# Performance work log

Measured on AMD Instinct MI355X. Metric: run time of the kernel, lower is better.

Reference implementation:

```python
import math
import jax, jax.numpy as jnp
import numpy as np

B, S, D, H = 4, 2048, 768, 12
HD = D // H  # 64


def setup_inputs() -> dict:
    key = jax.random.key(0)
    ks = jax.random.split(key, 10)
    sc = 0.02
    return {
        "hidden_states": jax.random.normal(ks[0], (B, S, D), dtype=jnp.float32),
        "attention_mask": jax.random.randint(ks[1], (1, H, S, S), 0, 2).astype(jnp.bool_),
        "q_w": jax.random.normal(ks[2], (D, D), dtype=jnp.float32) * sc,
        "q_b": jax.random.normal(ks[3], (D,), dtype=jnp.float32) * sc,
        "k_w": jax.random.normal(ks[4], (D, D), dtype=jnp.float32) * sc,
        "k_b": jax.random.normal(ks[5], (D,), dtype=jnp.float32) * sc,
        "v_w": jax.random.normal(ks[6], (D, D), dtype=jnp.float32) * sc,
        "v_b": jax.random.normal(ks[7], (D,), dtype=jnp.float32) * sc,
        "out_w": jax.random.normal(ks[8], (D, D), dtype=jnp.float32) * sc,
        "out_b": jax.random.normal(ks[9], (D,), dtype=jnp.float32) * sc,
    }


def _split_heads(x):
    # [B, S, D] -> [B, H, S, HD]
    b, s, _ = x.shape
    return x.reshape(b, s, H, HD).transpose(0, 2, 1, 3)


def reference(hidden_states, attention_mask, q_w, q_b, k_w, k_b, v_w, v_b, out_w, out_b):
    q = _split_heads(hidden_states @ q_w.T + q_b)
    k = _split_heads(hidden_states @ k_w.T + k_b)
    v = _split_heads(hidden_states @ v_w.T + v_b)
    scores = jnp.einsum("bhqd,bhkd->bhqk", q, k) / math.sqrt(HD)
    # prune_mode, before softmax: masked_fill(~mask, -inf)
    scores = jnp.where(attention_mask, scores, -jnp.inf)
    probs = jax.nn.softmax(scores, axis=-1)  # [B, H, S, S]
    ctx = jnp.einsum("bhqk,bhkd->bhqd", probs, v)
    ctx = ctx.transpose(0, 2, 1, 3).reshape(hidden_states.shape[0], -1, D)
    return ctx @ out_w.T + out_b
```

## Files before the change

kernel.cpp:

```cpp
#include <hip/hip_runtime.h>
#include <hip/hip_bf16.h>

#define B_ 4
#define S_ 2048
#define D_ 768
#define H_ 12
#define HD_ 64

typedef __attribute__((ext_vector_type(8))) short bf16x8;
typedef __attribute__((ext_vector_type(4))) float floatx4;

#define QSCALE 0.18033688011112042f

__device__ __forceinline__ unsigned short f2bf(float x) {
    union { float f; unsigned int u; } v; v.f = x;
    unsigned int r = v.u + 0x7fffu + ((v.u >> 16) & 1u);
    return (unsigned short)(r >> 16);
}

__device__ __forceinline__ unsigned int pk2bf(float a, float b) {
    __hip_bfloat162 h = __float22bfloat162_rn(make_float2(a, b));
    unsigned int u;
    __builtin_memcpy(&u, &h, 4);
    return u;
}

__device__ __forceinline__ void gload_lds16(const void* g, void* l) {
    __builtin_amdgcn_global_load_lds(
        (const __attribute__((address_space(1))) unsigned int*)g,
        (__attribute__((address_space(3))) unsigned int*)l, 16, 0, 0);
}

__global__ void prep(const float* __restrict__ hs,
                     const float* __restrict__ w0, const float* __restrict__ w1,
                     const float* __restrict__ w2, const float* __restrict__ w3,
                     const int* __restrict__ mask,
                     unsigned short* __restrict__ Xb,
                     unsigned short* __restrict__ Wb,
                     unsigned long long* __restrict__ bits) {
    int bid = blockIdx.x;
    int t = threadIdx.x;
    if (bid < 6144) {
        int i = bid * 256 + t;
        float4 f = ((const float4*)hs)[i];
        ushort4 o;
        o.x = f2bf(f.x); o.y = f2bf(f.y); o.z = f2bf(f.z); o.w = f2bf(f.w);
        ((ushort4*)Xb)[i] = o;
    } else if (bid < 8448) {
        int q = bid - 6144;
        int wid = q / 576;
        const float* src = (wid == 0) ? w0 : (wid == 1) ? w1 : (wid == 2) ? w2 : w3;
        unsigned short* d = Wb + (size_t)wid * 589824;
        int i = (q - wid * 576) * 256 + t;
        float4 f = ((const float4*)src)[i];
        ushort4 o;
        o.x = f2bf(f.x); o.y = f2bf(f.y); o.z = f2bf(f.z); o.w = f2bf(f.w);
        ((ushort4*)d)[i] = o;
    } else {
        size_t gw = ((size_t)(bid - 8448) * 256 + t) >> 6;
        int lane = t & 63;
        size_t base = gw * 256;
        unsigned long long b0 = __ballot(mask[base + lane] != 0);
        unsigned long long b1 = __ballot(mask[base + 64 + lane] != 0);
        unsigned long long b2 = __ballot(mask[base + 128 + lane] != 0);
        unsigned long long b3 = __ballot(mask[base + 192 + lane] != 0);
        if (lane == 0) {
            bits[gw * 4 + 0] = b0; bits[gw * 4 + 1] = b1;
            bits[gw * 4 + 2] = b2; bits[gw * 4 + 3] = b3;
        }
    }
}

__global__ __launch_bounds__(256) void qkv_gemm(
    const unsigned short* __restrict__ Xb,
    const unsigned short* __restrict__ Wq, const unsigned short* __restrict__ Wk,
    const unsigned short* __restrict__ Wv,
    const float* __restrict__ bq, const float* __restrict__ bk,
    const float* __restrict__ bv,
    unsigned short* __restrict__ Qo, unsigned short* __restrict__ Ko,
    unsigned short* __restrict__ Vo)
{
    const int z = blockIdx.z;
    const unsigned short* W = (z == 0) ? Wq : (z == 1) ? Wk : Wv;
    const float* bias = (z == 0) ? bq : (z == 1) ? bk : bv;
    unsigned short* Out = (z == 0) ? Qo : (z == 1) ? Ko : Vo;
    const float scale = (z == 0) ? QSCALE : 1.0f;

    const int m0 = blockIdx.x * 128;
    const int n0 = blockIdx.y * 128;

    __shared__ alignas(16) unsigned short SMall[16384];
    unsigned short* SM = SMall;

    const int t = threadIdx.x;
    const int lane = t & 63, w = t >> 6;
    const int c = lane & 15, quad = lane >> 4;
    const int wm = (w & 1) * 64, wn = (w >> 1) * 64;

    const int srowq = lane >> 2, sc8 = (lane & 3) * 8;

    floatx4 acc[4][4];
#pragma unroll
    for (int i = 0; i < 4; i++)
#pragma unroll
        for (int j = 0; j < 4; j++) acc[i][j] = (floatx4){0.f, 0.f, 0.f, 0.f};

#pragma unroll
    for (int i = 0; i < 2; i++) {
        int chunk = i * 4 + w;
        int row = chunk * 16 + srowq;
        gload_lds16(&Xb[(size_t)(m0 + row) * 768 + sc8], &SMall[chunk * 512]);
        gload_lds16(&W [(size_t)(n0 + row) * 768 + sc8], &SMall[4096 + chunk * 512]);
    }

    for (int it = 0; it < 24; it++) {
        const int cur = it & 1;
        __syncthreads();
        if (it + 1 < 24) {
            int k1 = (it + 1) * 32;
#pragma unroll
            for (int i = 0; i < 2; i++) {
                int chunk = i * 4 + w;
                int row = chunk * 16 + srowq;
                gload_lds16(&Xb[(size_t)(m0 + row) * 768 + k1 + sc8],
                            &SMall[(cur ^ 1) * 8192 + chunk * 512]);
                gload_lds16(&W [(size_t)(n0 + row) * 768 + k1 + sc8],
                            &SMall[(cur ^ 1) * 8192 + 4096 + chunk * 512]);
            }
        }
        const unsigned short* As = &SMall[cur * 8192];
        const unsigned short* Bs = As + 4096;
        bf16x8 a[4], b[4];
#pragma unroll
        for (int i = 0; i < 4; i++)
            a[i] = *(const bf16x8*)&As[(wm + i * 16 + c) * 32 + quad * 8];
#pragma unroll
        for (int j = 0; j < 4; j++)
            b[j] = *(const bf16x8*)&Bs[(wn + j * 16 + c) * 32 + quad * 8];
#pragma unroll
        for (int i = 0; i < 4; i++)
#pragma unroll
            for (int j = 0; j < 4; j++)
                acc[i][j] = __builtin_amdgcn_mfma_f32_16x16x32_bf16(
                    a[i], b[j], acc[i][j], 0, 0, 0);
    }
    __syncthreads();

    const int bb = m0 >> 11, ssb = m0 & 2047;
    if (z == 2) {
#pragma unroll
        for (int half = 0; half < 2; half++) {
            if ((w >> 1) == half) {
#pragma unroll
                for (int j = 0; j < 4; j++) {
                    int n_l = j * 16 + c;
                    float bias_n = bias[n0 + half * 64 + n_l];
#pragma unroll
                    for (int i = 0; i < 4; i++) {
#pragma unroll
                        for (int r = 0; r < 4; r++) {
                            int m = wm + i * 16 + quad * 4 + r;
                            int ms = m ^ (c << 3);
                            SM[n_l * 128 + ms] = f2bf(acc[i][j][r] + bias_n);
                        }
                    }
                }
            }
            __syncthreads();
#pragma unroll
            for (int rb = 0; rb < 2; rb++) {
                int n_l = (t >> 3) + rb * 32;
                int ch = t & 7;
                int n_abs = n0 + half * 64 + n_l;
                int hh = n_abs >> 6, dd = n_abs & 63;
                unsigned short* dst =
                    Out + (((size_t)(bb * H_ + hh)) * 64 + dd) * S_ + ssb;
#pragma unroll
                for (int p = 0; p < 2; p++) {
                    int mc = ch + p * 8;
                    uint4 v = *(const uint4*)&SM[n_l * 128 + ((mc ^ (n_l & 15)) * 8)];
                    *(uint4*)&dst[mc * 8] = v;
                }
            }
            __syncthreads();
        }
    } else {
#pragma unroll
        for (int half = 0; half < 2; half++) {
            if ((w >> 1) == half) {
#pragma unroll
                for (int j = 0; j < 4; j++) {
                    float bias_n = bias[n0 + half * 64 + j * 16 + c];
#pragma unroll
                    for (int i = 0; i < 4; i++) {
#pragma unroll
                        for (int r = 0; r < 4; r++) {
                            int m = wm + i * 16 + quad * 4 + r;
                            int chunk = (j * 2 + (c >> 3)) ^ ((m >> 1) & 7);
                            SM[m * 64 + chunk * 8 + (c & 7)] =
                                f2bf((acc[i][j][r] + bias_n) * scale);
                        }
                    }
                }
            }
            __syncthreads();
            {
                int hh = (n0 >> 6) + half;
                unsigned short* dst =
                    Out + ((size_t)(bb * H_ + hh) * S_ + ssb) * 64;
#pragma unroll
                for (int i = 0; i < 4; i++) {
                    int idx = i * 256 + t;
                    int m = idx >> 3, ch = idx & 7;
                    uint4 v = *(const uint4*)&SM[m * 64 + ((ch ^ ((m >> 1) & 7)) * 8)];
                    *(uint4*)&dst[(size_t)m * 64 + ch * 8] = v;
                }
            }
            __syncthreads();
        }
    }
}

__global__ __launch_bounds__(256) void out_gemm(
    const unsigned short* __restrict__ Cb, const unsigned short* __restrict__ Wo,
    const float* __restrict__ bo, float* __restrict__ out)
{
    const int m0 = blockIdx.x * 64;
    const int n0 = blockIdx.y * 128;

    __shared__ alignas(16) unsigned short SMall[12288];

    const int t = threadIdx.x;
    const int lane = t & 63, w = t >> 6;
    const int c = lane & 15, quad = lane >> 4;
    const int wm = (w & 1) * 32, wn = (w >> 1) * 64;

    const int arow = w * 16 + (lane >> 2);
    const int brow0 = (lane >> 2);
    const int sc8 = (lane & 3) * 8;

    floatx4 acc[2][4];
#pragma unroll
    for (int i = 0; i < 2; i++)
#pragma unroll
        for (int j = 0; j < 4; j++) acc[i][j] = (floatx4){0.f, 0.f, 0.f, 0.f};

    gload_lds16(&Cb[(size_t)(m0 + arow) * 768 + sc8], &SMall[w * 512]);
#pragma unroll
    for (int i = 0; i < 2; i++) {
        int chunk = i * 4 + w;
        gload_lds16(&Wo[(size_t)(n0 + chunk * 16 + brow0) * 768 + sc8],
                    &SMall[2048 + chunk * 512]);
    }

    for (int it = 0; it < 24; it++) {
        const int cur = it & 1;
        __syncthreads();
        if (it + 1 < 24) {
            int k1 = (it + 1) * 32;
            gload_lds16(&Cb[(size_t)(m0 + arow) * 768 + k1 + sc8],
                        &SMall[(cur ^ 1) * 6144 + w * 512]);
#pragma unroll
            for (int i = 0; i < 2; i++) {
                int chunk = i * 4 + w;
                gload_lds16(&Wo[(size_t)(n0 + chunk * 16 + brow0) * 768 + k1 + sc8],
                            &SMall[(cur ^ 1) * 6144 + 2048 + chunk * 512]);
            }
        }
        const unsigned short* As = &SMall[cur * 6144];
        const unsigned short* Bs = As + 2048;
        bf16x8 a[2], b[4];
#pragma unroll
        for (int i = 0; i < 2; i++)
            a[i] = *(const bf16x8*)&As[(wm + i * 16 + c) * 32 + quad * 8];
#pragma unroll
        for (int j = 0; j < 4; j++)
            b[j] = *(const bf16x8*)&Bs[(wn + j * 16 + c) * 32 + quad * 8];
#pragma unroll
        for (int i = 0; i < 2; i++)
#pragma unroll
            for (int j = 0; j < 4; j++)
                acc[i][j] = __builtin_amdgcn_mfma_f32_16x16x32_bf16(
                    a[i], b[j], acc[i][j], 0, 0, 0);
    }
    __syncthreads();

    float* SMf = (float*)SMall;
#pragma unroll
    for (int qtr = 0; qtr < 4; qtr++) {
        if ((w >> 1) == (qtr >> 1)) {
#pragma unroll
            for (int jj = 0; jj < 2; jj++) {
                int j = (qtr & 1) * 2 + jj;
                float bias_n = bo[n0 + wn + j * 16 + c];
                int chunk = jj * 4 + (c >> 2);
#pragma unroll
                for (int i = 0; i < 2; i++) {
#pragma unroll
                    for (int r = 0; r < 4; r++) {
                        int m = wm + i * 16 + quad * 4 + r;
                        SMf[m * 32 + ((chunk ^ (m & 7)) * 4) + (c & 3)] =
                            acc[i][j][r] + bias_n;
                    }
                }
            }
        }
        __syncthreads();
#pragma unroll
        for (int i = 0; i < 2; i++) {
            int idx = i * 256 + t;
            int m = idx >> 3, ch = idx & 7;
            float4 v = *(const float4*)&SMf[m * 32 + ((ch ^ (m & 7)) * 4)];
            *(float4*)&out[(size_t)(m0 + m) * 768 + n0 + qtr * 32 + ch * 4] = v;
        }
        __syncthreads();
    }
}

__global__ __launch_bounds__(256) void attn(
    const unsigned short* __restrict__ Q, const unsigned short* __restrict__ K,
    const unsigned short* __restrict__ Vt,
    const unsigned long long* __restrict__ mbits,
    unsigned short* __restrict__ ctx)
{
    const int lin = blockIdx.y * 16 + blockIdx.x;
    const int nn = (lin & 7) * 96 + (lin >> 3);
    const int qt = nn & 15;
    const int bh = nn >> 4;
    const int b = bh / H_, h = bh % H_;

    const unsigned short* Qp = Q + (size_t)bh * S_ * 64 + (size_t)qt * 128 * 64;
    const unsigned short* Kp = K + (size_t)bh * S_ * 64;
    const unsigned short* Vp = Vt + (size_t)bh * 64 * S_;

    __shared__ alignas(16) unsigned short Ks[2][64 * 64];
    __shared__ alignas(16) unsigned short Vs[2][64 * 64];
    __shared__ alignas(16) unsigned short Ps[4][16 * 64];

    const int t = threadIdx.x;
    const int lane = t & 63, w = t >> 6;
    const int c = lane & 15, quad = lane >> 4;

    bf16x8 aq[2][2];
#pragma unroll
    for (int st = 0; st < 2; st++) {
        aq[st][0] = *(const bf16x8*)&Qp[(size_t)(w * 32 + st * 16 + c) * 64 + quad * 8];
        aq[st][1] = *(const bf16x8*)&Qp[(size_t)(w * 32 + st * 16 + c) * 64 + 32 + quad * 8];
    }

    const unsigned long long* mrow =
        mbits + ((size_t)h * S_ + qt * 128 + w * 32 + quad * 4) * (S_ / 64);

    floatx4 acc_o[2][4];
#pragma unroll
    for (int st = 0; st < 2; st++)
#pragma unroll
        for (int i = 0; i < 4; i++) acc_o[st][i] = (floatx4){0.f, 0.f, 0.f, 0.f};
    float lp[2][4] = {{0.f, 0.f, 0.f, 0.f}, {0.f, 0.f, 0.f, 0.f}};

    const int srow = (lane >> 3);
    const int rc0 = ((quad     ) ^ (c & 7)) * 8;
    const int rc1 = ((quad + 4) ^ (c & 7)) * 8;

    const int psr0 = c * 64 + ((quad ^ (c & 7)) << 3);
    const int psr1 = c * 64 + (((quad + 4) ^ (c & 7)) << 3);

#pragma unroll
    for (int i = 0; i < 2; i++) {
        int chunk = i * 4 + w;
        int row = chunk * 8 + srow;
        int col8 = (((lane & 7) ^ ((row >> 2) & 7))) * 8;
        gload_lds16(&Kp[(size_t)row * 64 + col8], &Ks[0][chunk * 512]);
        gload_lds16(&Vp[(size_t)row * S_ + col8], &Vs[0][chunk * 512]);
    }

    for (int kt = 0; kt < S_ / 64; kt++) {
        const int cur = kt & 1;
        __syncthreads();

        unsigned long long mk[2][4];
#pragma unroll
        for (int st = 0; st < 2; st++)
#pragma unroll
            for (int r = 0; r < 4; r++)
                mk[st][r] = mrow[st * 512 + r * 32 + kt];

        if (kt + 1 < S_ / 64) {
#pragma unroll
            for (int i = 0; i < 2; i++) {
                int chunk = i * 4 + w;
                int row = chunk * 8 + srow;
                int col8 = (((lane & 7) ^ ((row >> 2) & 7))) * 8;
                gload_lds16(&Kp[(size_t)((kt + 1) * 64 + row) * 64 + col8],
                            &Ks[cur ^ 1][chunk * 512]);
                gload_lds16(&Vp[(size_t)row * S_ + (kt + 1) * 64 + col8],
                            &Vs[cur ^ 1][chunk * 512]);
            }
        }

        unsigned int pk1[2][4];
#pragma unroll
        for (int p = 0; p < 2; p++) {
            floatx4 zz[2][2];
            zz[0][0] = (floatx4){0.f, 0.f, 0.f, 0.f};
            zz[0][1] = (floatx4){0.f, 0.f, 0.f, 0.f};
            zz[1][0] = (floatx4){0.f, 0.f, 0.f, 0.f};
            zz[1][1] = (floatx4){0.f, 0.f, 0.f, 0.f};
#pragma unroll
            for (int q2 = 0; q2 < 2; q2++) {
                int kr = 4 * c + 2 * p + q2;
                bf16x8 bk0 = *(const bf16x8*)&Ks[cur][kr * 64 + rc0];
                bf16x8 bk1 = *(const bf16x8*)&Ks[cur][kr * 64 + rc1];
                zz[0][q2] = __builtin_amdgcn_mfma_f32_16x16x32_bf16(aq[0][0], bk0, zz[0][q2], 0, 0, 0);
                zz[0][q2] = __builtin_amdgcn_mfma_f32_16x16x32_bf16(aq[0][1], bk1, zz[0][q2], 0, 0, 0);
                zz[1][q2] = __builtin_amdgcn_mfma_f32_16x16x32_bf16(aq[1][0], bk0, zz[1][q2], 0, 0, 0);
                zz[1][q2] = __builtin_amdgcn_mfma_f32_16x16x32_bf16(aq[1][1], bk1, zz[1][q2], 0, 0, 0);
            }

            asm volatile("" ::: "memory");
#pragma unroll
            for (int r = 0; r < 4; r++) {
                unsigned int n2 = (unsigned int)(mk[0][r] >> (4 * c + 2 * p)) & 3u;
                float p0 = (n2 & 1u) ? __builtin_amdgcn_exp2f(zz[0][0][r]) : 0.f;
                float p1 = (n2 & 2u) ? __builtin_amdgcn_exp2f(zz[0][1][r]) : 0.f;
                lp[0][r] += p0 + p1;
                int row = quad * 4 + r;
                *(unsigned int*)&Ps[w][row * 64 + (((c >> 1) ^ (row & 7)) << 3) +
                                       ((c & 1) << 2) + 2 * p] = pk2bf(p0, p1);
            }
#pragma unroll
            for (int r = 0; r < 4; r++) {
                unsigned int n2 = (unsigned int)(mk[1][r] >> (4 * c + 2 * p)) & 3u;
                float p0 = (n2 & 1u) ? __builtin_amdgcn_exp2f(zz[1][0][r]) : 0.f;
                float p1 = (n2 & 2u) ? __builtin_amdgcn_exp2f(zz[1][1][r]) : 0.f;
                lp[1][r] += p0 + p1;
                pk1[p][r] = pk2bf(p0, p1);
            }
            asm volatile("" ::: "memory");
        }

        bf16x8 ap[2][2];
        ap[0][0] = *(const bf16x8*)&Ps[w][psr0];
        ap[0][1] = *(const bf16x8*)&Ps[w][psr1];
        asm volatile("" ::: "memory");
#pragma unroll
        for (int p = 0; p < 2; p++)
#pragma unroll
            for (int r = 0; r < 4; r++) {
                int row = quad * 4 + r;
                *(unsigned int*)&Ps[w][row * 64 + (((c >> 1) ^ (row & 7)) << 3) +
                                       ((c & 1) << 2) + 2 * p] = pk1[p][r];
            }
        asm volatile("" ::: "memory");
        ap[1][0] = *(const bf16x8*)&Ps[w][psr0];
        ap[1][1] = *(const bf16x8*)&Ps[w][psr1];

#pragma unroll
        for (int nt = 0; nt < 4; nt++) {
            int vr = 4 * c + nt;
            bf16x8 bv0 = *(const bf16x8*)&Vs[cur][vr * 64 + rc0];
            bf16x8 bv1 = *(const bf16x8*)&Vs[cur][vr * 64 + rc1];
#pragma unroll
            for (int st = 0; st < 2; st++) {
                acc_o[st][nt] = __builtin_amdgcn_mfma_f32_16x16x32_bf16(ap[st][0], bv0, acc_o[st][nt], 0, 0, 0);
                acc_o[st][nt] = __builtin_amdgcn_mfma_f32_16x16x32_bf16(ap[st][1], bv1, acc_o[st][nt], 0, 0, 0);
            }
        }
    }

#pragma unroll
    for (int st = 0; st < 2; st++)
#pragma unroll
        for (int r = 0; r < 4; r++) {
            float s = lp[st][r];
#pragma unroll
            for (int o = 1; o < 16; o <<= 1) s += __shfl_xor(s, o, 64);
            lp[st][r] = s;
        }

#pragma unroll
    for (int st = 0; st < 2; st++)
#pragma unroll
        for (int nt = 0; nt < 4; nt++)
#pragma unroll
            for (int r = 0; r < 4; r++) {
                int qrow = qt * 128 + w * 32 + st * 16 + quad * 4 + r;
                int dd = 4 * c + nt;
                float v = acc_o[st][nt][r] / lp[st][r];
                ctx[((size_t)b * S_ + qrow) * 768 + h * 64 + dd] = f2bf(v);
            }
}

extern "C" void kernel_launch(void* const* d_in, const int* in_sizes, int n_in,
                              void* d_out, int out_size, void* d_ws, size_t ws_size,
                              hipStream_t stream) {
    const float* hs    = (const float*)d_in[0];
    const int*   mask  = (const int*)d_in[1];
    const float* q_w   = (const float*)d_in[2];
    const float* q_b   = (const float*)d_in[3];
    const float* k_w   = (const float*)d_in[4];
    const float* k_b   = (const float*)d_in[5];
    const float* v_w   = (const float*)d_in[6];
    const float* v_b   = (const float*)d_in[7];
    const float* out_w = (const float*)d_in[8];
    const float* out_b = (const float*)d_in[9];
    float* out = (float*)d_out;

    unsigned short* Xb  = (unsigned short*)d_ws;
    unsigned short* Wqb = Xb + 6291456;
    unsigned short* Wkb = Wqb + 589824;
    unsigned short* Wvb = Wkb + 589824;
    unsigned short* Wob = Wvb + 589824;
    unsigned short* Qb  = Wob + 589824;
    unsigned short* Kb  = Qb + 6291456;
    unsigned short* Vtb = Kb + 6291456;
    unsigned short* Cb  = Vtb + 6291456;
    unsigned long long* mbits = (unsigned long long*)(Cb + 6291456);

    prep<<<57600, 256, 0, stream>>>(hs, q_w, k_w, v_w, out_w, mask, Xb, Wqb, mbits);
    qkv_gemm<<<dim3(64, 6, 3), 256, 0, stream>>>(Xb, Wqb, Wkb, Wvb,
                                                 q_b, k_b, v_b, Qb, Kb, Vtb);
    attn<<<dim3(16, 48), 256, 0, stream>>>(Qb, Kb, Vtb, mbits, Cb);
    out_gemm<<<dim3(128, 6), 256, 0, stream>>>(Cb, Wob, out_b, out);
}
```

Measured before the change: 470.0 us.

## Move mask bit-packing into QKV GEMM launch to overlap with compute

Mask bit-packing leaves the prep kernel and moves into the QKV GEMM kernel. One of every four blocks now packs a slice of the mask while the other three run GEMM tiles, using a flattened 1D grid of 1536 blocks. The aim is to overlap the memory-bound mask read with the compute-bound GEMM instead of running them one after the other. This risks load imbalance, since the 384 mask blocks each loop over 128 iterations and may run longer than the GEMM tiles.

```diff
diff --git a/kernel.cpp b/kernel.cpp
--- a/kernel.cpp
+++ b/kernel.cpp
@@ -34,10 +34,8 @@
 __global__ void prep(const float* __restrict__ hs,
                      const float* __restrict__ w0, const float* __restrict__ w1,
                      const float* __restrict__ w2, const float* __restrict__ w3,
-                     const int* __restrict__ mask,
                      unsigned short* __restrict__ Xb,
-                     unsigned short* __restrict__ Wb,
-                     unsigned long long* __restrict__ bits) {
+                     unsigned short* __restrict__ Wb) {
     int bid = blockIdx.x;
     int t = threadIdx.x;
     if (bid < 6144) {
@@ -46,7 +44,7 @@
         ushort4 o;
         o.x = f2bf(f.x); o.y = f2bf(f.y); o.z = f2bf(f.z); o.w = f2bf(f.w);
         ((ushort4*)Xb)[i] = o;
-    } else if (bid < 8448) {
+    } else {
         int q = bid - 6144;
         int wid = q / 576;
         const float* src = (wid == 0) ? w0 : (wid == 1) ? w1 : (wid == 2) ? w2 : w3;
@@ -56,18 +54,6 @@
         ushort4 o;
         o.x = f2bf(f.x); o.y = f2bf(f.y); o.z = f2bf(f.z); o.w = f2bf(f.w);
         ((ushort4*)d)[i] = o;
-    } else {
-        size_t gw = ((size_t)(bid - 8448) * 256 + t) >> 6;
-        int lane = t & 63;
-        size_t base = gw * 256;
-        unsigned long long b0 = __ballot(mask[base + lane] != 0);
-        unsigned long long b1 = __ballot(mask[base + 64 + lane] != 0);
-        unsigned long long b2 = __ballot(mask[base + 128 + lane] != 0);
-        unsigned long long b3 = __ballot(mask[base + 192 + lane] != 0);
-        if (lane == 0) {
-            bits[gw * 4 + 0] = b0; bits[gw * 4 + 1] = b1;
-            bits[gw * 4 + 2] = b2; bits[gw * 4 + 3] = b3;
-        }
     }
 }
 
@@ -78,21 +64,45 @@
     const float* __restrict__ bq, const float* __restrict__ bk,
     const float* __restrict__ bv,
     unsigned short* __restrict__ Qo, unsigned short* __restrict__ Ko,
-    unsigned short* __restrict__ Vo)
+    unsigned short* __restrict__ Vo,
+    const int* __restrict__ mask,
+    unsigned long long* __restrict__ bits)
 {
-    const int z = blockIdx.z;
+    const int bid = blockIdx.x;
+    const int t = threadIdx.x;
+
+    if ((bid & 3) == 3) {
+        const int mi = bid >> 2;
+        const int lane = t & 63, wv = t >> 6;
+        for (int it = 0; it < 128; ++it) {
+            size_t gw = (size_t)mi * 512 + it * 4 + wv;
+            size_t base = gw * 256;
+            unsigned long long b0 = __ballot(mask[base + lane] != 0);
+            unsigned long long b1 = __ballot(mask[base + 64 + lane] != 0);
+            unsigned long long b2 = __ballot(mask[base + 128 + lane] != 0);
+            unsigned long long b3 = __ballot(mask[base + 192 + lane] != 0);
+            if (lane == 0) {
+                bits[gw * 4 + 0] = b0; bits[gw * 4 + 1] = b1;
+                bits[gw * 4 + 2] = b2; bits[gw * 4 + 3] = b3;
+            }
+        }
+        return;
+    }
+
+    const int qid = (bid >> 2) * 3 + (bid & 3);
+    const int z = qid / 384;
+    const int rest = qid % 384;
+    const int m0 = (rest % 64) * 128;
+    const int n0 = (rest / 64) * 128;
+
     const unsigned short* W = (z == 0) ? Wq : (z == 1) ? Wk : Wv;
     const float* bias = (z == 0) ? bq : (z == 1) ? bk : bv;
     unsigned short* Out = (z == 0) ? Qo : (z == 1) ? Ko : Vo;
     const float scale = (z == 0) ? QSCALE : 1.0f;
 
-    const int m0 = blockIdx.x * 128;
-    const int n0 = blockIdx.y * 128;
-
     __shared__ alignas(16) unsigned short SMall[16384];
     unsigned short* SM = SMall;
 
-    const int t = threadIdx.x;
     const int lane = t & 63, w = t >> 6;
     const int c = lane & 15, quad = lane >> 4;
     const int wm = (w & 1) * 64, wn = (w >> 1) * 64;
@@ -517,9 +527,10 @@
     unsigned short* Cb  = Vtb + 6291456;
     unsigned long long* mbits = (unsigned long long*)(Cb + 6291456);
 
-    prep<<<57600, 256, 0, stream>>>(hs, q_w, k_w, v_w, out_w, mask, Xb, Wqb, mbits);
-    qkv_gemm<<<dim3(64, 6, 3), 256, 0, stream>>>(Xb, Wqb, Wkb, Wvb,
-                                                 q_b, k_b, v_b, Qb, Kb, Vtb);
+    prep<<<8448, 256, 0, stream>>>(hs, q_w, k_w, v_w, out_w, Xb, Wqb);
+    qkv_gemm<<<1536, 256, 0, stream>>>(Xb, Wqb, Wkb, Wvb,
+                                       q_b, k_b, v_b, Qb, Kb, Vtb,
+                                       mask, mbits);
     attn<<<dim3(16, 48), 256, 0, stream>>>(Qb, Kb, Vtb, mbits, Cb);
     out_gemm<<<dim3(128, 6), 256, 0, stream>>>(Cb, Wob, out_b, out);
 }
```

New measurement: 615.8 us. 31.0% more time.
